# Optimization experiments

Measured on AMD Instinct MI355X. Metric: run time of the kernel, lower is better.

Reference implementation:

```python
import jax, jax.numpy as jnp
import numpy as np
from itertools import combinations

F = 24                 # num_fields
VOCAB_PER_FIELD = 10000
D = 16                 # embed_dim
B = 2048               # batch
FIELD_DIMS = [VOCAB_PER_FIELD] * F
TOTAL_VOCAB = sum(FIELD_DIMS)
# FeaturesEmbedding/FeaturesLinear offsets: cumulative field dims
OFFSETS = np.concatenate(([0], np.cumsum(FIELD_DIMS)[:-1])).astype(np.int64)  # (F,)
PAIRS = np.array(list(combinations(range(F), 2)), dtype=np.int64)   # (276, 2)
TRIPS = np.array(list(combinations(range(F), 3)), dtype=np.int64)   # (2024, 3)


def setup_inputs() -> dict:
    key = jax.random.key(0)
    k0, k1, k2, k3, k4 = jax.random.split(key, 5)
    x = jax.random.randint(k0, (B, F), 0, VOCAB_PER_FIELD)
    embed_table = jax.random.normal(k1, (TOTAL_VOCAB, D), dtype=jnp.float32) * 0.01
    lin_weight = jax.random.normal(k2, (TOTAL_VOCAB, 1), dtype=jnp.float32) * 0.01
    lin_bias = jnp.zeros((1,), dtype=jnp.float32)
    genotype_2nd = jax.random.normal(k3, (PAIRS.shape[0], 1), dtype=jnp.float32)
    genotype_3rd = jax.random.normal(k4, (TRIPS.shape[0], 1), dtype=jnp.float32)
    return {
        "x": x,
        "embed_table": embed_table,
        "lin_weight": lin_weight,
        "lin_bias": lin_bias,
        "genotype_2nd": genotype_2nd,
        "genotype_3rd": genotype_3rd,
    }


def reference(x, embed_table, lin_weight, lin_bias, genotype_2nd, genotype_3rd):
    idx = x + jnp.asarray(OFFSETS)[None, :]            # (B, F) global ids
    emb = embed_table[idx]                             # (B, F, D)
    # genotype is detached in the original forward
    g2 = jax.lax.stop_gradient(genotype_2nd)[:, 0]     # (P,)
    g3 = jax.lax.stop_gradient(genotype_3rd)[:, 0]     # (T,)
    # 2nd-order gated interactions: sum_t sum_d g2[t] * e_i * e_j
    p = emb[:, PAIRS[:, 0]]                            # (B, P, D)
    q = emb[:, PAIRS[:, 1]]
    nasfm_2nd = jnp.einsum('bpd,bpd,p->b', p, q, g2)   # (B,)
    # 3rd-order gated interactions
    p1 = emb[:, TRIPS[:, 0]]                           # (B, T, D)
    q1 = emb[:, TRIPS[:, 1]]
    r1 = emb[:, TRIPS[:, 2]]
    nasfm_3rd = jnp.einsum('btd,btd,btd,t->b', p1, q1, r1, g3)  # (B,)
    # FeaturesLinear: sum of per-feature weights + bias
    linear = jnp.sum(lin_weight[idx][..., 0], axis=1) + lin_bias[0]  # (B,)
    return jax.nn.sigmoid(linear + nasfm_2nd + nasfm_3rd)
```

## Files before the change

### kernel.cpp

```cpp
#include <hip/hip_runtime.h>
#include <math.h>

#define F 24
#define D 16
#define BATCH 2048
#define NPAIR 276
#define NTRIP 2024
#define VOCAB 10000
#define SLAB 392
#define LONG_SLOTS 80
#define SHORT_SLOTS 224
#define LONG_F (LONG_SLOTS * 28)
#define CW_FLOATS (LONG_F + SHORT_SLOTS * 16)

__host__ __device__ constexpr int pair_base(int i) { return i * 23 - i * (i - 1) / 2; }
__host__ __device__ constexpr int trip_base(int i) {
    return NTRIP - (24 - i) * (23 - i) * (22 - i) / 6;
}
__host__ __device__ constexpr int trip_idx(int i, int j, int k) {
    return trip_base(i) + (j - i - 1) * (46 - i - j) / 2 + (k - j - 1);
}
__device__ __forceinline__ int lbase(int i) { return 11 * i - i * (i - 1) / 2; }
__device__ __forceinline__ int sbase(int i) { return 144 + (35 - i) * (i - 12) / 2; }

__global__ __launch_bounds__(256) void repack_kernel(const float* __restrict__ g2,
                                                     const float* __restrict__ g3,
                                                     float* __restrict__ cw) {
    const int t = blockIdx.x * 256 + threadIdx.x;
    if (t >= CW_FLOATS) return;
    float v = 0.f;
    if (t < LONG_F) {
        const int slot = t / 28, field = t - slot * 28;
        if (slot < 66) {
            int i = 0;
            while (lbase(i + 1) <= slot) ++i;
            const int j = i + 1 + (slot - lbase(i));
            if (field == 0) v = __int_as_float(i);
            else if (field == 1) v = __int_as_float(j);
            else if (field == 2) v = g2[pair_base(i) + (j - i - 1)];
            else if (field >= 4) {
                const int k = field - 4;
                if (k > j) v = g3[trip_idx(i, j, k)];
            }
        }
    } else {
        const int tt = t - LONG_F;
        const int slot = tt / 16, field = tt - slot * 16;
        if (slot < 210) {
            int i, j;
            if (slot < 144) { i = slot / 12; j = 12 + (slot - 12 * i); }
            else { i = 12; while (sbase(i + 1) <= slot) ++i; j = i + 1 + (slot - sbase(i)); }
            if (field == 0) v = __int_as_float(i);
            else if (field == 1) v = __int_as_float(j);
            else if (field == 2) v = g2[pair_base(i) + (j - i - 1)];
            else if (field >= 3 && field <= 13) {
                const int k = 10 + field;
                if (k > j) v = g3[trip_idx(i, j, k)];
            }
        }
    }
    cw[t] = v;
}

__global__ __launch_bounds__(1024, 4) void ctr_main(
    const int* __restrict__ x, const float* __restrict__ emb,
    const float* __restrict__ lw, const float* __restrict__ lb,
    const float* __restrict__ cw, float* __restrict__ out) {
    __shared__ float s_e[4 * SLAB];
    __shared__ float s_lw[4 * F];
    __shared__ float s_part[16][4];

    const int tid = threadIdx.x;
    const int row0 = blockIdx.x * 4;

    if (tid < 4 * F * 4) {
        const int seg = tid >> 2, q = tid & 3;
        const int r = seg / F, f = seg - r * F;
        const int idx = x[(row0 + r) * F + f] + f * VOCAB;
        float4 v = reinterpret_cast<const float4*>(emb)[idx * 4 + q];
        float* b = &s_e[r * SLAB + f * D + q * 4];
        b[0] = v.x; b[1] = v.y; b[2] = v.z; b[3] = v.w;
    } else if (tid < 4 * F * 4 + 4 * F) {
        const int tt = tid - 4 * F * 4;
        const int r = tt / F, f = tt - r * F;
        s_lw[tt] = lw[x[(row0 + r) * F + f] + f * VOCAB];
    }
    __syncthreads();

    const int d = tid & 15;
    const int r = (tid >> 4) & 3;
    const int w = __builtin_amdgcn_readfirstlane(tid >> 6);
    const float* se = &s_e[r * SLAB];

    float e[F];
#pragma unroll
    for (int f = 0; f < F; ++f) e[f] = se[f * D + d];

    float acc = 0.f;

    const float4* Lp = reinterpret_cast<const float4*>(cw) + w * (5 * 7);
#pragma unroll 2
    for (int s = 0; s < 5; ++s) {
        float4 h  = Lp[s * 7 + 0];
        float4 c0 = Lp[s * 7 + 1], c1 = Lp[s * 7 + 2], c2 = Lp[s * 7 + 3];
        float4 c3 = Lp[s * 7 + 4], c4 = Lp[s * 7 + 5], c5 = Lp[s * 7 + 6];
        int i = __float_as_int(h.x), j = __float_as_int(h.y);
        float ei = se[i * D + d];
        float ej = se[j * D + d];
        float ta = h.z, tb = 0.f;
        ta = fmaf(c0.z, e[2],  ta); tb = fmaf(c0.w, e[3],  tb);
        ta = fmaf(c1.x, e[4],  ta); tb = fmaf(c1.y, e[5],  tb);
        ta = fmaf(c1.z, e[6],  ta); tb = fmaf(c1.w, e[7],  tb);
        ta = fmaf(c2.x, e[8],  ta); tb = fmaf(c2.y, e[9],  tb);
        ta = fmaf(c2.z, e[10], ta); tb = fmaf(c2.w, e[11], tb);
        ta = fmaf(c3.x, e[12], ta); tb = fmaf(c3.y, e[13], tb);
        ta = fmaf(c3.z, e[14], ta); tb = fmaf(c3.w, e[15], tb);
        ta = fmaf(c4.x, e[16], ta); tb = fmaf(c4.y, e[17], tb);
        ta = fmaf(c4.z, e[18], ta); tb = fmaf(c4.w, e[19], tb);
        ta = fmaf(c5.x, e[20], ta); tb = fmaf(c5.y, e[21], tb);
        ta = fmaf(c5.z, e[22], ta); tb = fmaf(c5.w, e[23], tb);
        acc = fmaf(ei * ej, ta + tb, acc);
    }

    const float4* Sp = reinterpret_cast<const float4*>(cw) + (LONG_F / 4) + w * (14 * 4);
#pragma unroll 2
    for (int s = 0; s < 14; ++s) {
        float4 h  = Sp[s * 4 + 0];
        float4 k0 = Sp[s * 4 + 1], k1 = Sp[s * 4 + 2], k2 = Sp[s * 4 + 3];
        int i = __float_as_int(h.x), j = __float_as_int(h.y);
        float ei = se[i * D + d];
        float ej = se[j * D + d];
        float ta = h.z, tb = 0.f;
        ta = fmaf(h.w,  e[13], ta);
        tb = fmaf(k0.x, e[14], tb); ta = fmaf(k0.y, e[15], ta);
        tb = fmaf(k0.z, e[16], tb); ta = fmaf(k0.w, e[17], ta);
        tb = fmaf(k1.x, e[18], tb); ta = fmaf(k1.y, e[19], ta);
        tb = fmaf(k1.z, e[20], tb); ta = fmaf(k1.w, e[21], ta);
        tb = fmaf(k2.x, e[22], tb); ta = fmaf(k2.y, e[23], ta);
        acc = fmaf(ei * ej, ta + tb, acc);
    }

#pragma unroll
    for (int m = 1; m < 16; m <<= 1) acc += __shfl_xor(acc, m, 64);
    if (d == 0) s_part[w][r] = acc;
    __syncthreads();

    if (tid < 64) {
        const int rr = tid >> 4, c = tid & 15;
        float v = s_part[c][rr];
#pragma unroll
        for (int m = 1; m < 16; m <<= 1) v += __shfl_xor(v, m, 64);
        if (c == 0) {
            float lin = lb[0];
#pragma unroll
            for (int f = 0; f < F; ++f) lin += s_lw[rr * F + f];
            float z = v + lin;
            out[row0 + rr] = 1.f / (1.f + __expf(-z));
        }
    }
}

extern "C" void kernel_launch(void* const* d_in, const int* in_sizes, int n_in,
                              void* d_out, int out_size, void* d_ws, size_t ws_size,
                              hipStream_t stream) {
    const int*   x   = (const int*)d_in[0];
    const float* emb = (const float*)d_in[1];
    const float* lw  = (const float*)d_in[2];
    const float* lb  = (const float*)d_in[3];
    const float* g2  = (const float*)d_in[4];
    const float* g3  = (const float*)d_in[5];
    float* out = (float*)d_out;
    float* cw  = (float*)d_ws;

    hipLaunchKernelGGL(repack_kernel, dim3((CW_FLOATS + 255) / 256), dim3(256), 0, stream,
                       g2, g3, cw);
    hipLaunchKernelGGL(ctr_main, dim3(BATCH / 4), dim3(1024), 0, stream,
                       x, emb, lw, lb, cw, out);
}
```

Measured before the change: 17.16 us.

## Transpose shared embedding slab to d-major and reuse e_i across slots

Stores each row's embeddings in shared memory as d-major with a padded stride of 28, so each lane loads its 24 field values with six float4 reads instead of 24 scalar reads. The repacked weight table gains a flag per slot that marks whether i matches the previous slot, letting the kernel skip reloading e_i from shared memory. This cuts LDS instruction count, at the cost of a larger padded slab, a data-dependent branch, and a somewhat more complex repack kernel.

```diff
diff --git a/kernel.cpp b/kernel.cpp
--- a/kernel.cpp
+++ b/kernel.cpp
@@ -7,7 +7,7 @@
 #define NPAIR 276
 #define NTRIP 2024
 #define VOCAB 10000
-#define SLAB 392
+#define SLAB 456
 #define LONG_SLOTS 80
 #define SHORT_SLOTS 224
 #define LONG_F (LONG_SLOTS * 28)
@@ -22,6 +22,20 @@
 }
 __device__ __forceinline__ int lbase(int i) { return 11 * i - i * (i - 1) / 2; }
 __device__ __forceinline__ int sbase(int i) { return 144 + (35 - i) * (i - 12) / 2; }
+
+__device__ __forceinline__ void ij_of_long(int q, int& i, int& j) {
+    if (q >= 66) { i = 0; j = 0; return; }
+    i = 0;
+    while (lbase(i + 1) <= q) ++i;
+    j = i + 1 + (q - lbase(i));
+}
+__device__ __forceinline__ void ij_of_short(int q, int& i, int& j) {
+    if (q >= 210) { i = 0; j = 0; return; }
+    if (q < 144) { i = q / 12; j = 12 + (q - 12 * i); return; }
+    i = 12;
+    while (sbase(i + 1) <= q) ++i;
+    j = i + 1 + (q - sbase(i));
+}
 
 __global__ __launch_bounds__(256) void repack_kernel(const float* __restrict__ g2,
                                                      const float* __restrict__ g3,
@@ -31,32 +45,34 @@
     float v = 0.f;
     if (t < LONG_F) {
         const int slot = t / 28, field = t - slot * 28;
-        if (slot < 66) {
-            int i = 0;
-            while (lbase(i + 1) <= slot) ++i;
-            const int j = i + 1 + (slot - lbase(i));
-            if (field == 0) v = __int_as_float(i);
-            else if (field == 1) v = __int_as_float(j);
-            else if (field == 2) v = g2[pair_base(i) + (j - i - 1)];
-            else if (field >= 4) {
-                const int k = field - 4;
-                if (k > j) v = g3[trip_idx(i, j, k)];
-            }
+        int i, j;
+        ij_of_long(slot, i, j);
+        const bool real = slot < 66;
+        if (field == 0) v = __int_as_float(i);
+        else if (field == 1) v = __int_as_float(j);
+        else if (field == 2) { if (real) v = g2[pair_base(i) + (j - i - 1)]; }
+        else if (field == 3) {
+            int ip, jp;
+            if (slot % 5 != 0) { ij_of_long(slot - 1, ip, jp); if (ip == i) v = __int_as_float(1); }
+        } else {
+            const int k = field - 4;
+            if (real && k > j) v = g3[trip_idx(i, j, k)];
         }
     } else {
         const int tt = t - LONG_F;
         const int slot = tt / 16, field = tt - slot * 16;
-        if (slot < 210) {
-            int i, j;
-            if (slot < 144) { i = slot / 12; j = 12 + (slot - 12 * i); }
-            else { i = 12; while (sbase(i + 1) <= slot) ++i; j = i + 1 + (slot - sbase(i)); }
-            if (field == 0) v = __int_as_float(i);
-            else if (field == 1) v = __int_as_float(j);
-            else if (field == 2) v = g2[pair_base(i) + (j - i - 1)];
-            else if (field >= 3 && field <= 13) {
-                const int k = 10 + field;
-                if (k > j) v = g3[trip_idx(i, j, k)];
-            }
+        int i, j;
+        ij_of_short(slot, i, j);
+        const bool real = slot < 210;
+        if (field == 0) v = __int_as_float(i);
+        else if (field == 1) v = __int_as_float(j);
+        else if (field == 2) { if (real) v = g2[pair_base(i) + (j - i - 1)]; }
+        else if (field >= 3 && field <= 13) {
+            const int k = 10 + field;
+            if (real && k > j) v = g3[trip_idx(i, j, k)];
+        } else if (field == 15) {
+            int ip, jp;
+            if (slot % 14 != 0) { ij_of_short(slot - 1, ip, jp); if (ip == i) v = __int_as_float(1); }
         }
     }
     cw[t] = v;
@@ -78,8 +94,11 @@
         const int r = seg / F, f = seg - r * F;
         const int idx = x[(row0 + r) * F + f] + f * VOCAB;
         float4 v = reinterpret_cast<const float4*>(emb)[idx * 4 + q];
-        float* b = &s_e[r * SLAB + f * D + q * 4];
-        b[0] = v.x; b[1] = v.y; b[2] = v.z; b[3] = v.w;
+        float* b = &s_e[r * SLAB + f];
+        b[(q * 4 + 0) * 28] = v.x;
+        b[(q * 4 + 1) * 28] = v.y;
+        b[(q * 4 + 2) * 28] = v.z;
+        b[(q * 4 + 3) * 28] = v.w;
     } else if (tid < 4 * F * 4 + 4 * F) {
         const int tt = tid - 4 * F * 4;
         const int r = tt / F, f = tt - r * F;
@@ -90,23 +109,30 @@
     const int d = tid & 15;
     const int r = (tid >> 4) & 3;
     const int w = __builtin_amdgcn_readfirstlane(tid >> 6);
-    const float* se = &s_e[r * SLAB];
+    const float* sed = &s_e[r * SLAB + d * 28];
 
     float e[F];
-#pragma unroll
-    for (int f = 0; f < F; ++f) e[f] = se[f * D + d];
+    {
+        const float4* se4 = reinterpret_cast<const float4*>(sed);
+#pragma unroll
+        for (int n = 0; n < 6; ++n) {
+            float4 v = se4[n];
+            e[4 * n] = v.x; e[4 * n + 1] = v.y; e[4 * n + 2] = v.z; e[4 * n + 3] = v.w;
+        }
+    }
 
     float acc = 0.f;
 
     const float4* Lp = reinterpret_cast<const float4*>(cw) + w * (5 * 7);
+    float eiL = 0.f;
 #pragma unroll 2
     for (int s = 0; s < 5; ++s) {
         float4 h  = Lp[s * 7 + 0];
         float4 c0 = Lp[s * 7 + 1], c1 = Lp[s * 7 + 2], c2 = Lp[s * 7 + 3];
         float4 c3 = Lp[s * 7 + 4], c4 = Lp[s * 7 + 5], c5 = Lp[s * 7 + 6];
         int i = __float_as_int(h.x), j = __float_as_int(h.y);
-        float ei = se[i * D + d];
-        float ej = se[j * D + d];
+        if (!__float_as_int(h.w)) eiL = sed[i];
+        float ej = sed[j];
         float ta = h.z, tb = 0.f;
         ta = fmaf(c0.z, e[2],  ta); tb = fmaf(c0.w, e[3],  tb);
         ta = fmaf(c1.x, e[4],  ta); tb = fmaf(c1.y, e[5],  tb);
@@ -119,17 +145,18 @@
         ta = fmaf(c4.z, e[18], ta); tb = fmaf(c4.w, e[19], tb);
         ta = fmaf(c5.x, e[20], ta); tb = fmaf(c5.y, e[21], tb);
         ta = fmaf(c5.z, e[22], ta); tb = fmaf(c5.w, e[23], tb);
-        acc = fmaf(ei * ej, ta + tb, acc);
+        acc = fmaf(eiL * ej, ta + tb, acc);
     }
 
     const float4* Sp = reinterpret_cast<const float4*>(cw) + (LONG_F / 4) + w * (14 * 4);
+    float eiS = 0.f;
 #pragma unroll 2
     for (int s = 0; s < 14; ++s) {
         float4 h  = Sp[s * 4 + 0];
         float4 k0 = Sp[s * 4 + 1], k1 = Sp[s * 4 + 2], k2 = Sp[s * 4 + 3];
         int i = __float_as_int(h.x), j = __float_as_int(h.y);
-        float ei = se[i * D + d];
-        float ej = se[j * D + d];
+        if (!__float_as_int(k2.w)) eiS = sed[i];
+        float ej = sed[j];
         float ta = h.z, tb = 0.f;
         ta = fmaf(h.w,  e[13], ta);
         tb = fmaf(k0.x, e[14], tb); ta = fmaf(k0.y, e[15], ta);
@@ -137,7 +164,7 @@
         tb = fmaf(k1.x, e[18], tb); ta = fmaf(k1.y, e[19], ta);
         tb = fmaf(k1.z, e[20], tb); ta = fmaf(k1.w, e[21], ta);
         tb = fmaf(k2.x, e[22], tb); ta = fmaf(k2.y, e[23], ta);
-        acc = fmaf(ei * ej, ta + tb, acc);
+        acc = fmaf(eiS * ej, ta + tb, acc);
     }
 
 #pragma unroll
```

After: 19.58 us. 1.14x slower.
